# Kernel tuning notes

Measured on AMD Instinct MI355X. Metric: run time of the kernel, lower is better.

Reference implementation:

```python
import jax, jax.numpy as jnp
import numpy as np

MARGIN = 0.35


def setup_inputs() -> dict:
    key = jax.random.key(0)
    k1, k2 = jax.random.split(key)
    N, D = 8192, 512
    inp = jax.random.normal(k1, (N, D), dtype=jnp.float32)
    label = jax.random.randint(k2, (N,), 0, D, dtype=jnp.int64)
    return {"input": inp, "label": label}


def reference(input, label):
    N = input.shape[0]
    # Faithful to the torch code: squared-norm terms use L2-normalized input,
    # but the -2*x@x.T cross term uses the UNnormalized input (original quirk).
    x_norm = input / jnp.linalg.norm(input, axis=1, keepdims=True)
    sq = jnp.sum(x_norm * x_norm, axis=1, keepdims=True)  # [N,1]
    dist = sq + sq.T - 2.0 * (input @ input.T)            # [N,N]
    mask = label[:, None] == label[None, :]               # same-label mask
    neg_inf = jnp.array(-jnp.inf, dist.dtype)
    pos_inf = jnp.array(jnp.inf, dist.dtype)
    # hardest positive (max over same-label), hardest negative (min over diff-label)
    positive_part = jnp.max(jnp.where(mask, dist, neg_inf), axis=1)
    negative_part = jnp.min(jnp.where(mask, pos_inf, dist), axis=1)
    triplet = jnp.mean(jnp.maximum(positive_part - negative_part + MARGIN, 0.0))
    # cross entropy: input are logits, label class indices
    logz = jax.nn.logsumexp(input, axis=1)
    true_logit = jnp.take_along_axis(input, label[:, None].astype(jnp.int32), axis=1)[:, 0]
    ce = jnp.mean(logz - true_logit)
    return triplet + ce
```

## Files before the change

### kernel.cpp

```cpp
#include <hip/hip_runtime.h>
#include <hip/hip_bf16.h>
#include <stdint.h>

#define N_ROWS 8192
#define DIM 512
#define NLAB 512
#define MARGIN_F 0.35f
#define NBLK 64
#define NPURE 1953
#define NDIAG 127
#define NTILE (NPURE + NDIAG)
#define ROWSTAT_BLOCKS (N_ROWS / 4)

typedef __attribute__((ext_vector_type(4))) float floatx4;
typedef __attribute__((ext_vector_type(8))) int intx8;

__device__ __forceinline__ unsigned enc_f(float f) {
    unsigned u = __float_as_uint(f);
    return (u & 0x80000000u) ? ~u : (u | 0x80000000u);
}
__device__ __forceinline__ float dec_f(unsigned e) {
    unsigned u = (e & 0x80000000u) ? (e ^ 0x80000000u) : ~e;
    return __uint_as_float(u);
}

__device__ __forceinline__ void load_lds16(const void* g, void* l) {
    __builtin_amdgcn_global_load_lds((__attribute__((address_space(1))) void*)(void*)g,
                                     (__attribute__((address_space(3))) void*)l, 16, 0, 0);
}

__device__ __forceinline__ float rowmax16(float x) {
    int v, y;
    v = __float_as_int(x);
    y = __builtin_amdgcn_update_dpp(v, v, 0x121, 0xf, 0xf, true);
    x = fmaxf(x, __int_as_float(y)); v = __float_as_int(x);
    y = __builtin_amdgcn_update_dpp(v, v, 0x122, 0xf, 0xf, true);
    x = fmaxf(x, __int_as_float(y)); v = __float_as_int(x);
    y = __builtin_amdgcn_update_dpp(v, v, 0x124, 0xf, 0xf, true);
    x = fmaxf(x, __int_as_float(y)); v = __float_as_int(x);
    y = __builtin_amdgcn_update_dpp(v, v, 0x128, 0xf, 0xf, true);
    return fmaxf(x, __int_as_float(y));
}
__device__ __forceinline__ float rowmin16(float x) {
    int v, y;
    v = __float_as_int(x);
    y = __builtin_amdgcn_update_dpp(v, v, 0x121, 0xf, 0xf, true);
    x = fminf(x, __int_as_float(y)); v = __float_as_int(x);
    y = __builtin_amdgcn_update_dpp(v, v, 0x122, 0xf, 0xf, true);
    x = fminf(x, __int_as_float(y)); v = __float_as_int(x);
    y = __builtin_amdgcn_update_dpp(v, v, 0x124, 0xf, 0xf, true);
    x = fminf(x, __int_as_float(y)); v = __float_as_int(x);
    y = __builtin_amdgcn_update_dpp(v, v, 0x128, 0xf, 0xf, true);
    return fminf(x, __int_as_float(y));
}

__global__ __launch_bounds__(512) void histscan_kernel(const int* __restrict__ label,
                                                       int* __restrict__ offsetArr,
                                                       int* __restrict__ cnt,
                                                       float* __restrict__ out) {
    __shared__ int h[NLAB];
    __shared__ int sc[NLAB];
    int t = threadIdx.x;
    h[t] = 0;
    __syncthreads();
    for (int i = t; i < N_ROWS; i += 512) atomicAdd(&h[label[i]], 1);
    __syncthreads();
    int v = h[t];
    sc[t] = v;
    __syncthreads();
    for (int d = 1; d < NLAB; d <<= 1) {
        int add = (t >= d) ? sc[t - d] : 0;
        __syncthreads();
        sc[t] += add;
        __syncthreads();
    }
    offsetArr[t] = sc[t] - v;
    cnt[t] = 0;
    if (t == 0) out[0] = 0.f;
}

__global__ __launch_bounds__(256) void rowstats_kernel(const float* __restrict__ x,
                                                       const int* __restrict__ label,
                                                       const int* __restrict__ offsetArr,
                                                       int* __restrict__ cnt,
                                                       unsigned char* __restrict__ a8,
                                                       int* __restrict__ sortedLabel,
                                                       float* __restrict__ cePartial,
                                                       unsigned* __restrict__ minEnc,
                                                       unsigned* __restrict__ maxEnc) {
    int gid = blockIdx.x * 256 + threadIdx.x;
    if (gid < N_ROWS) { minEnc[gid] = 0xFFFFFFFFu; maxEnc[gid] = 0u; }

    int w = threadIdx.x >> 6;
    int row = blockIdx.x * 4 + w;
    int l = threadIdx.x & 63;
    const float* xr = x + (size_t)row * DIM;
    float4 v0 = ((const float4*)xr)[2 * l];
    float4 v1 = ((const float4*)xr)[2 * l + 1];
    float vals[8] = {v0.x, v0.y, v0.z, v0.w, v1.x, v1.y, v1.z, v1.w};

    float mx = vals[0];
#pragma unroll
    for (int i = 1; i < 8; i++) mx = fmaxf(mx, vals[i]);
#pragma unroll
    for (int s = 1; s < 64; s <<= 1) mx = fmaxf(mx, __shfl_xor(mx, s, 64));

    float se = 0.f;
#pragma unroll
    for (int i = 0; i < 8; i++) se += expf(vals[i] - mx);
#pragma unroll
    for (int s = 1; s < 64; s <<= 1) se += __shfl_xor(se, s, 64);

    int pos = 0;
    if (l == 0) {
        int lab = label[row];
        pos = offsetArr[lab] + atomicAdd(&cnt[lab], 1);
        sortedLabel[pos] = lab;
    }
    pos = __shfl(pos, 0, 64);

    int w0 = __builtin_amdgcn_cvt_pk_fp8_f32(vals[0], vals[1], 0, false);
    w0 = __builtin_amdgcn_cvt_pk_fp8_f32(vals[2], vals[3], w0, true);
    int w1 = __builtin_amdgcn_cvt_pk_fp8_f32(vals[4], vals[5], 0, false);
    w1 = __builtin_amdgcn_cvt_pk_fp8_f32(vals[6], vals[7], w1, true);
    ((uint2*)(a8 + (size_t)pos * DIM))[l] = make_uint2((unsigned)w0, (unsigned)w1);

    __shared__ float wsum[4];
    if (l == 0) {
        float tl = xr[label[row]];
        wsum[w] = mx + logf(se) - tl;
    }
    __syncthreads();
    if (threadIdx.x == 0)
        cePartial[blockIdx.x] = wsum[0] + wsum[1] + wsum[2] + wsum[3];
}

__global__ __launch_bounds__(256, 3) void gemm_kernel(const unsigned char* __restrict__ A,
                                                      const int* __restrict__ sortedLabel,
                                                      unsigned* __restrict__ minEnc,
                                                      unsigned* __restrict__ maxEnc) {
    __shared__ unsigned char As[128 * 128];
    __shared__ unsigned char Bs[128 * 128];
    __shared__ float redA[128][2];
    __shared__ float redB[128][8];

    int b = blockIdx.x;
    bool diag = (b < NDIAG);
    int bi, bj;
    if (diag) {
        bi = (b < 64) ? b : (b - 63);
        bj = (b < 64) ? b : (b - 64);
    } else {
        int p = b - NDIAG;
        int ci = (int)((sqrtf(8.0f * (float)p + 1.0f) - 1.0f) * 0.5f);
        while ((ci + 1) * (ci + 2) / 2 <= p) ci++;
        while (ci * (ci + 1) / 2 > p) ci--;
        bj = p - ci * (ci + 1) / 2;
        bi = ci + 2;
    }
    int ibase = bi * 128, jbase = bj * 128;

    int t = threadIdx.x;
    int w = t >> 6, l = t & 63;
    int wm = w >> 1, wn = w & 1;
    int q = l >> 4, lm = l & 15;

    floatx4 acc[4][4];
#pragma unroll
    for (int a = 0; a < 4; a++)
#pragma unroll
        for (int c = 0; c < 4; c++) acc[a][c] = (floatx4)0.f;

    int s_r = t >> 3;
    int s_c = ((t & 7) ^ (s_r & 7));

    for (int kk = 0; kk < 4; kk++) {
        int k0 = kk * 128;
#pragma unroll
        for (int i2 = 0; i2 < 4; i2++) {
            int r = i2 * 32 + s_r;
            int slot = (i2 * 256 + t) * 16;
            load_lds16(A + (size_t)(ibase + r) * DIM + k0 + s_c * 16, As + slot);
            load_lds16(A + (size_t)(jbase + r) * DIM + k0 + s_c * 16, Bs + slot);
        }
        __syncthreads();

        intx8 bfv[4];
#pragma unroll
        for (int tn = 0; tn < 4; tn++) {
            int R = wn * 64 + tn * 16 + lm;
            const int4* rowp = (const int4*)(Bs + R * 128);
            int4 lo = rowp[(2 * q) ^ (R & 7)];
            int4 hi = rowp[(2 * q + 1) ^ (R & 7)];
            intx8 v;
            v[0] = lo.x; v[1] = lo.y; v[2] = lo.z; v[3] = lo.w;
            v[4] = hi.x; v[5] = hi.y; v[6] = hi.z; v[7] = hi.w;
            bfv[tn] = v;
        }
#pragma unroll
        for (int tm = 0; tm < 4; tm++) {
            int R = wm * 64 + tm * 16 + lm;
            const int4* rowp = (const int4*)(As + R * 128);
            int4 lo = rowp[(2 * q) ^ (R & 7)];
            int4 hi = rowp[(2 * q + 1) ^ (R & 7)];
            intx8 af;
            af[0] = lo.x; af[1] = lo.y; af[2] = lo.z; af[3] = lo.w;
            af[4] = hi.x; af[5] = hi.y; af[6] = hi.z; af[7] = hi.w;
#pragma unroll
            for (int tn = 0; tn < 4; tn++)
                acc[tm][tn] = __builtin_amdgcn_mfma_scale_f32_16x16x128_f8f6f4(
                    af, bfv[tn], acc[tm][tn], 0, 0,
                    0, 0x7F7F7F7F,
                    0, 0x7F7F7F7F);
        }
        __syncthreads();
    }

    const float INF = __builtin_inff();

    if (!diag) {
        float mxJ[4];
#pragma unroll
        for (int tn = 0; tn < 4; tn++) mxJ[tn] = -INF;
#pragma unroll
        for (int tm = 0; tm < 4; tm++) {
#pragma unroll
            for (int r = 0; r < 4; r++) {
                int row_l = wm * 64 + tm * 16 + q * 4 + r;
                float mxI = -INF;
#pragma unroll
                for (int tn = 0; tn < 4; tn++) {
                    float v = acc[tm][tn][r];
                    mxI = fmaxf(mxI, v);
                    mxJ[tn] = fmaxf(mxJ[tn], v);
                }
                mxI = rowmax16(mxI);
                if (lm == 0) redA[row_l][wn] = mxI;
            }
        }
#pragma unroll
        for (int tn = 0; tn < 4; tn++)
            redB[wn * 64 + tn * 16 + lm][wm * 4 + q] = mxJ[tn];
        __syncthreads();
        if (t < 128) {
            atomicMax(&maxEnc[ibase + t], enc_f(fmaxf(redA[t][0], redA[t][1])));
            float vj = redB[t][0];
#pragma unroll
            for (int s = 1; s < 8; s++) vj = fmaxf(vj, redB[t][s]);
            atomicMax(&maxEnc[jbase + t], enc_f(vj));
        }
    } else {
        int* labi = (int*)As;
        int* labj = labi + 128;
        float (*redImn)[2] = (float (*)[2])(labj + 128);
        float (*redJmn)[8] = (float (*)[8])(redImn + 128);
        if (t < 128) labi[t] = sortedLabel[ibase + t];
        else labj[t - 128] = sortedLabel[jbase + t - 128];
        __syncthreads();

        int jlab[4];
#pragma unroll
        for (int tn = 0; tn < 4; tn++) jlab[tn] = labj[wn * 64 + tn * 16 + lm];

        float mnJ[4], mxJ[4];
#pragma unroll
        for (int tn = 0; tn < 4; tn++) { mnJ[tn] = INF; mxJ[tn] = -INF; }

#pragma unroll
        for (int tm = 0; tm < 4; tm++) {
#pragma unroll
            for (int r = 0; r < 4; r++) {
                int row_l = wm * 64 + tm * 16 + q * 4 + r;
                int il = labi[row_l];
                float mnI = INF, mxI = -INF;
#pragma unroll
                for (int tn = 0; tn < 4; tn++) {
                    float v = acc[tm][tn][r];
                    bool same = (jlab[tn] == il);
                    float vs = same ? v : INF;
                    float vd = same ? -INF : v;
                    mnI = fminf(mnI, vs);
                    mxI = fmaxf(mxI, vd);
                    mnJ[tn] = fminf(mnJ[tn], vs);
                    mxJ[tn] = fmaxf(mxJ[tn], vd);
                }
                mnI = rowmin16(mnI);
                mxI = rowmax16(mxI);
                if (lm == 0) { redImn[row_l][wn] = mnI; redA[row_l][wn] = mxI; }
            }
        }
#pragma unroll
        for (int tn = 0; tn < 4; tn++) {
            int col_l = wn * 64 + tn * 16 + lm;
            redJmn[col_l][wm * 4 + q] = mnJ[tn];
            redB[col_l][wm * 4 + q] = mxJ[tn];
        }
        __syncthreads();
        if (t < 128) {
            atomicMin(&minEnc[ibase + t], enc_f(fminf(redImn[t][0], redImn[t][1])));
            atomicMax(&maxEnc[ibase + t], enc_f(fmaxf(redA[t][0], redA[t][1])));
            float vjm = redJmn[t][0], vjx = redB[t][0];
#pragma unroll
            for (int s = 1; s < 8; s++) {
                vjm = fminf(vjm, redJmn[t][s]);
                vjx = fmaxf(vjx, redB[t][s]);
            }
            atomicMin(&minEnc[jbase + t], enc_f(vjm));
            atomicMax(&maxEnc[jbase + t], enc_f(vjx));
        }
    }
}

__global__ __launch_bounds__(256) void finalize_kernel(const unsigned* __restrict__ minEnc,
                                                       const unsigned* __restrict__ maxEnc,
                                                       const float* __restrict__ cePartial,
                                                       float* __restrict__ out) {
    int gid = blockIdx.x * 256 + threadIdx.x;
    float mn = dec_f(minEnc[gid]);
    float mxv = dec_f(maxEnc[gid]);
    float s = fmaxf(2.0f * (mxv - mn) + MARGIN_F, 0.f);
    if (gid < ROWSTAT_BLOCKS) s += cePartial[gid];
#pragma unroll
    for (int sh = 1; sh < 64; sh <<= 1) s += __shfl_xor(s, sh, 64);
    __shared__ float red[4];
    int w = threadIdx.x >> 6, l = threadIdx.x & 63;
    if (l == 0) red[w] = s;
    __syncthreads();
    if (threadIdx.x == 0)
        atomicAdd(out, (red[0] + red[1] + red[2] + red[3]) * (1.0f / (float)N_ROWS));
}

extern "C" void kernel_launch(void* const* d_in, const int* in_sizes, int n_in,
                              void* d_out, int out_size, void* d_ws, size_t ws_size,
                              hipStream_t stream) {
    const float* x = (const float*)d_in[0];
    const int* label = (const int*)d_in[1];
    float* out = (float*)d_out;

    char* ws = (char*)d_ws;
    unsigned char* a8 = (unsigned char*)ws;
    char* p = ws + (size_t)N_ROWS * DIM;
    unsigned* minEnc = (unsigned*)p;            p += N_ROWS * 4;
    unsigned* maxEnc = (unsigned*)p;            p += N_ROWS * 4;
    float* cePartial = (float*)p;               p += ROWSTAT_BLOCKS * 4;
    int* offsetArr = (int*)p;                   p += NLAB * 4;
    int* cnt = (int*)p;                         p += NLAB * 4;
    int* sortedLabel = (int*)p;                 p += N_ROWS * 4;

    histscan_kernel<<<1, 512, 0, stream>>>(label, offsetArr, cnt, out);
    rowstats_kernel<<<ROWSTAT_BLOCKS, 256, 0, stream>>>(x, label, offsetArr, cnt, a8,
                                                        sortedLabel, cePartial, minEnc, maxEnc);
    gemm_kernel<<<NTILE, 256, 0, stream>>>(a8, sortedLabel, minEnc, maxEnc);
    finalize_kernel<<<32, 256, 0, stream>>>(minEnc, maxEnc, cePartial, out);
}
```

Measured before the change: 103.5 us.

## Fuse finalize into GEMM via last-block reduction and split atomics across threads

Removes the separate finalize kernel launch. The last GEMM tile to finish, detected with a global atomic counter and threadfences, now does the final triplet plus cross-entropy reduction. It also spreads the row and column atomic updates over all 256 threads instead of 128. This saves one launch and its gap, at the cost of a serialized tail reduction done by a single block.

```diff
diff --git a/kernel.cpp b/kernel.cpp
--- a/kernel.cpp
+++ b/kernel.cpp
@@ -57,7 +57,8 @@
 __global__ __launch_bounds__(512) void histscan_kernel(const int* __restrict__ label,
                                                        int* __restrict__ offsetArr,
                                                        int* __restrict__ cnt,
-                                                       float* __restrict__ out) {
+                                                       float* __restrict__ out,
+                                                       unsigned* __restrict__ tileCnt) {
     __shared__ int h[NLAB];
     __shared__ int sc[NLAB];
     int t = threadIdx.x;
@@ -76,7 +77,7 @@
     }
     offsetArr[t] = sc[t] - v;
     cnt[t] = 0;
-    if (t == 0) out[0] = 0.f;
+    if (t == 0) { out[0] = 0.f; tileCnt[0] = 0u; }
 }
 
 __global__ __launch_bounds__(256) void rowstats_kernel(const float* __restrict__ x,
@@ -138,7 +139,10 @@
 __global__ __launch_bounds__(256, 3) void gemm_kernel(const unsigned char* __restrict__ A,
                                                       const int* __restrict__ sortedLabel,
                                                       unsigned* __restrict__ minEnc,
-                                                      unsigned* __restrict__ maxEnc) {
+                                                      unsigned* __restrict__ maxEnc,
+                                                      const float* __restrict__ cePartial,
+                                                      float* __restrict__ out,
+                                                      unsigned* __restrict__ tileCnt) {
     __shared__ unsigned char As[128 * 128];
     __shared__ unsigned char Bs[128 * 128];
     __shared__ float redA[128][2];
@@ -244,10 +248,12 @@
         __syncthreads();
         if (t < 128) {
             atomicMax(&maxEnc[ibase + t], enc_f(fmaxf(redA[t][0], redA[t][1])));
-            float vj = redB[t][0];
-#pragma unroll
-            for (int s = 1; s < 8; s++) vj = fmaxf(vj, redB[t][s]);
-            atomicMax(&maxEnc[jbase + t], enc_f(vj));
+        } else {
+            int u = t - 128;
+            float vj = redB[u][0];
+#pragma unroll
+            for (int s = 1; s < 8; s++) vj = fmaxf(vj, redB[u][s]);
+            atomicMax(&maxEnc[jbase + u], enc_f(vj));
         }
     } else {
         int* labi = (int*)As;
@@ -299,35 +305,44 @@
         if (t < 128) {
             atomicMin(&minEnc[ibase + t], enc_f(fminf(redImn[t][0], redImn[t][1])));
             atomicMax(&maxEnc[ibase + t], enc_f(fmaxf(redA[t][0], redA[t][1])));
-            float vjm = redJmn[t][0], vjx = redB[t][0];
+        } else {
+            int u = t - 128;
+            float vjm = redJmn[u][0], vjx = redB[u][0];
 #pragma unroll
             for (int s = 1; s < 8; s++) {
-                vjm = fminf(vjm, redJmn[t][s]);
-                vjx = fmaxf(vjx, redB[t][s]);
+                vjm = fminf(vjm, redJmn[u][s]);
+                vjx = fmaxf(vjx, redB[u][s]);
             }
-            atomicMin(&minEnc[jbase + t], enc_f(vjm));
-            atomicMax(&maxEnc[jbase + t], enc_f(vjx));
-        }
-    }
-}
-
-__global__ __launch_bounds__(256) void finalize_kernel(const unsigned* __restrict__ minEnc,
-                                                       const unsigned* __restrict__ maxEnc,
-                                                       const float* __restrict__ cePartial,
-                                                       float* __restrict__ out) {
-    int gid = blockIdx.x * 256 + threadIdx.x;
-    float mn = dec_f(minEnc[gid]);
-    float mxv = dec_f(maxEnc[gid]);
-    float s = fmaxf(2.0f * (mxv - mn) + MARGIN_F, 0.f);
-    if (gid < ROWSTAT_BLOCKS) s += cePartial[gid];
-#pragma unroll
-    for (int sh = 1; sh < 64; sh <<= 1) s += __shfl_xor(s, sh, 64);
-    __shared__ float red[4];
-    int w = threadIdx.x >> 6, l = threadIdx.x & 63;
-    if (l == 0) red[w] = s;
-    __syncthreads();
-    if (threadIdx.x == 0)
-        atomicAdd(out, (red[0] + red[1] + red[2] + red[3]) * (1.0f / (float)N_ROWS));
+            atomicMin(&minEnc[jbase + u], enc_f(vjm));
+            atomicMax(&maxEnc[jbase + u], enc_f(vjx));
+        }
+    }
+
+    __shared__ int lastFlag;
+    __threadfence();
+    if (t == 0) {
+        unsigned prev = atomicAdd(tileCnt, 1u);
+        lastFlag = (prev == (unsigned)(NTILE - 1));
+    }
+    __syncthreads();
+    if (lastFlag) {
+        __threadfence();
+        float s = 0.f;
+        for (int i = t; i < N_ROWS; i += 256) {
+            float mn = dec_f(minEnc[i]);
+            float mxv = dec_f(maxEnc[i]);
+            float v = fmaxf(2.0f * (mxv - mn) + MARGIN_F, 0.f);
+            if (i < ROWSTAT_BLOCKS) v += cePartial[i];
+            s += v;
+        }
+#pragma unroll
+        for (int sh = 1; sh < 64; sh <<= 1) s += __shfl_xor(s, sh, 64);
+        __shared__ float red[4];
+        if (l == 0) red[w] = s;
+        __syncthreads();
+        if (t == 0)
+            out[0] = (red[0] + red[1] + red[2] + red[3]) * (1.0f / (float)N_ROWS);
+    }
 }
 
 extern "C" void kernel_launch(void* const* d_in, const int* in_sizes, int n_in,
@@ -346,10 +361,11 @@
     int* offsetArr = (int*)p;                   p += NLAB * 4;
     int* cnt = (int*)p;                         p += NLAB * 4;
     int* sortedLabel = (int*)p;                 p += N_ROWS * 4;
-
-    histscan_kernel<<<1, 512, 0, stream>>>(label, offsetArr, cnt, out);
+    unsigned* tileCnt = (unsigned*)p;           p += 64;
+
+    histscan_kernel<<<1, 512, 0, stream>>>(label, offsetArr, cnt, out, tileCnt);
     rowstats_kernel<<<ROWSTAT_BLOCKS, 256, 0, stream>>>(x, label, offsetArr, cnt, a8,
                                                         sortedLabel, cePartial, minEnc, maxEnc);
-    gemm_kernel<<<NTILE, 256, 0, stream>>>(a8, sortedLabel, minEnc, maxEnc);
-    finalize_kernel<<<32, 256, 0, stream>>>(minEnc, maxEnc, cePartial, out);
-}
+    gemm_kernel<<<NTILE, 256, 0, stream>>>(a8, sortedLabel, minEnc, maxEnc,
+                                           cePartial, out, tileCnt);
+}
```

Result: slower. 229.1 us (+121.3%).
